# Performance work log

Hardware: AMD Instinct MI355X
Metric: run time of the kernel (lower is better)

## Reference

```python
import jax, jax.numpy as jnp
import numpy as np


def setup_inputs() -> dict:
    key = jax.random.key(0)
    k1, k2, k3, k4, k5, k6 = jax.random.split(key, 6)
    n_vars = 1000000
    n_constrs = 500000
    nnz = 20000000
    pred = jax.random.normal(k1, (n_vars,), dtype=jnp.float32)
    constr_idx = jax.random.randint(k2, (nnz,), 0, n_constrs, dtype=jnp.int32)
    var_idx = jax.random.randint(k3, (nnz,), 0, n_vars, dtype=jnp.int32)
    coeff = jax.random.normal(k4, (nnz,), dtype=jnp.float32)
    constr_rhs = jax.random.normal(k5, (n_constrs,), dtype=jnp.float32)
    constr_sense = jax.random.randint(k6, (n_constrs,), 1, 4, dtype=jnp.int32)  # 1=<=, 2=>=, 3===
    return {
        "pred": pred,
        "constr_idx": constr_idx,
        "var_idx": var_idx,
        "coeff": coeff,
        "constr_rhs": constr_rhs,
        "constr_sense": constr_sense,
        "n_vars": n_vars,
        "n_constrs": n_constrs,
    }


def reference(pred, constr_idx, var_idx, coeff, constr_rhs, constr_sense, n_vars, n_constrs):
    # probs = sigmoid(pred); ax[i] = sum over nnz entries of coeff * probs[var_idx]
    probs = jax.nn.sigmoid(pred)
    contrib = coeff * probs[var_idx]                      # [nnz]
    ax = jax.ops.segment_sum(contrib, constr_idx, num_segments=n_constrs)  # [n_constrs]
    le = jax.nn.relu(ax - constr_rhs)      # sense == 1 (<=)
    ge = jax.nn.relu(constr_rhs - ax)      # sense == 2 (>=)
    eq = jnp.abs(ax - constr_rhs)          # sense == 3 (==)
    violations = jnp.where(constr_sense == 1, le,
                  jnp.where(constr_sense == 2, ge,
                   jnp.where(constr_sense == 3, eq, jnp.zeros_like(ax))))
    return violations.mean()  # reduction='mean'
```

## Files before the change

### kernel.cpp

```cpp
#include <hip/hip_runtime.h>
#include <math.h>

#define R_LOG2 13
#define R_BKT  8192
#define SLICE  8
#define MAXNB  64
#define PB     512
#define BLK_RECS 8192

typedef int      iv4 __attribute__((ext_vector_type(4)));
typedef float    fv4 __attribute__((ext_vector_type(4)));
typedef unsigned uv4 __attribute__((ext_vector_type(4)));

__device__ __forceinline__ unsigned short f32_to_bf16_rne(float f) {
    unsigned b = __builtin_bit_cast(unsigned, f);
    b += 0x7FFFu + ((b >> 16) & 1u);
    return (unsigned short)(b >> 16);
}


__global__ void init_fast(const float4* __restrict__ pred4,
                          ushort4* __restrict__ probs4,
                          float4* __restrict__ ax4,
                          unsigned* __restrict__ cursor,
                          float* __restrict__ out,
                          int n_vars4, int nc4, int nb) {
    int i = blockIdx.x * blockDim.x + threadIdx.x;
    if (i < n_vars4) {
        float4 p = pred4[i];
        ushort4 q;
        q.x = f32_to_bf16_rne(1.0f / (1.0f + expf(-p.x)));
        q.y = f32_to_bf16_rne(1.0f / (1.0f + expf(-p.y)));
        q.z = f32_to_bf16_rne(1.0f / (1.0f + expf(-p.z)));
        q.w = f32_to_bf16_rne(1.0f / (1.0f + expf(-p.w)));
        probs4[i] = q;
    }
    if (i < nc4) ax4[i] = make_float4(0.f, 0.f, 0.f, 0.f);
    if (i < nb) cursor[i] = 0;
    if (i == 0) out[0] = 0.0f;
}

__global__ __launch_bounds__(PB) void partition_kernel(
        const int* __restrict__ cidx, const int* __restrict__ vidx,
        const float* __restrict__ coeff, const unsigned short* __restrict__ probs,
        unsigned* __restrict__ cursor, unsigned* __restrict__ recs,
        int nnz4, int nb, unsigned cap) {
    __shared__ unsigned sorted[BLK_RECS];
    __shared__ unsigned hist[8 * MAXNB];
    __shared__ unsigned lcur[8 * MAXNB];
    __shared__ unsigned bst[MAXNB + 1];
    __shared__ unsigned gbs[MAXNB];

    const int tid  = threadIdx.x;
    const int w    = tid >> 6;
    const int lane = tid & 63;

    hist[tid] = 0;

    unsigned rw[16];
    unsigned bk[16];
    bool     gv[4];
    const unsigned vbase = blockIdx.x * (BLK_RECS / 4);
    const bool full = (vbase + (BLK_RECS / 4)) <= (unsigned)nnz4;

    if (full) {
        #pragma unroll
        for (int g = 0; g < 4; ++g) {
            unsigned v = vbase + g * PB + (unsigned)tid;
            iv4 c4 = __builtin_nontemporal_load((const iv4*)cidx + v);
            iv4 v4 = __builtin_nontemporal_load((const iv4*)vidx + v);
            fv4 w4 = __builtin_nontemporal_load((const fv4*)coeff + v);
            int   cc[4] = {c4.x, c4.y, c4.z, c4.w};
            float vv[4] = {
                w4.x * __builtin_bit_cast(float, (unsigned)probs[v4.x] << 16),
                w4.y * __builtin_bit_cast(float, (unsigned)probs[v4.y] << 16),
                w4.z * __builtin_bit_cast(float, (unsigned)probs[v4.z] << 16),
                w4.w * __builtin_bit_cast(float, (unsigned)probs[v4.w] << 16)};
            #pragma unroll
            for (int j = 0; j < 4; ++j) {
                int k = g * 4 + j;
                unsigned bits = __builtin_bit_cast(unsigned, vv[j]);
                bits += 0x7FFFu + ((bits >> 16) & 1u);
                rw[k] = ((unsigned)(cc[j] & (R_BKT - 1)) << 16) | (bits >> 16);
                bk[k] = (unsigned)cc[j] >> R_LOG2;
            }
            gv[g] = true;
        }
    } else {
        #pragma unroll
        for (int g = 0; g < 4; ++g) {
            unsigned v = vbase + g * PB + (unsigned)tid;
            gv[g] = v < (unsigned)nnz4;
            if (gv[g]) {
                int4   c4 = ((const int4*)cidx)[v];
                int4   v4 = ((const int4*)vidx)[v];
                float4 w4 = ((const float4*)coeff)[v];
                int   cc[4] = {c4.x, c4.y, c4.z, c4.w};
                float vv[4] = {
                    w4.x * __builtin_bit_cast(float, (unsigned)probs[v4.x] << 16),
                    w4.y * __builtin_bit_cast(float, (unsigned)probs[v4.y] << 16),
                    w4.z * __builtin_bit_cast(float, (unsigned)probs[v4.z] << 16),
                    w4.w * __builtin_bit_cast(float, (unsigned)probs[v4.w] << 16)};
                #pragma unroll
                for (int j = 0; j < 4; ++j) {
                    int k = g * 4 + j;
                    unsigned bits = __builtin_bit_cast(unsigned, vv[j]);
                    bits += 0x7FFFu + ((bits >> 16) & 1u);
                    rw[k] = ((unsigned)(cc[j] & (R_BKT - 1)) << 16) | (bits >> 16);
                    bk[k] = (unsigned)cc[j] >> R_LOG2;
                }
            }
        }
    }
    __syncthreads();

    if (full) {
        #pragma unroll
        for (int k = 0; k < 16; ++k)
            atomicAdd(&hist[(w << 6) + bk[k]], 1u);
    } else {
        #pragma unroll
        for (int g = 0; g < 4; ++g) if (gv[g]) {
            #pragma unroll
            for (int j = 0; j < 4; ++j)
                atomicAdd(&hist[(w << 6) + bk[g * 4 + j]], 1u);
        }
    }
    __syncthreads();

    if (w == 0) {
        unsigned h[8];
        unsigned cnt = 0;
        if (lane < nb) {
            #pragma unroll
            for (int j = 0; j < 8; ++j) { h[j] = hist[(j << 6) + lane]; cnt += h[j]; }
        }
        unsigned sc = cnt;
        #pragma unroll
        for (int d = 1; d < 64; d <<= 1) {
            unsigned t = __shfl_up(sc, d, 64);
            if (lane >= d) sc += t;
        }
        unsigned excl  = sc - cnt;
        unsigned total = __shfl(sc, nb - 1, 64);
        if (lane < nb) {
            bst[lane] = excl;
            unsigned run = excl;
            #pragma unroll
            for (int j = 0; j < 8; ++j) { lcur[(j << 6) + lane] = run; run += h[j]; }
            gbs[lane] = cnt ? atomicAdd(&cursor[lane], cnt) : 0u;
        }
        if (lane == 0) bst[nb] = total;
    }
    __syncthreads();

    if (full) {
        #pragma unroll
        for (int k = 0; k < 16; ++k) {
            unsigned pos = atomicAdd(&lcur[(w << 6) + bk[k]], 1u);
            sorted[pos] = rw[k];
        }
    } else {
        #pragma unroll
        for (int g = 0; g < 4; ++g) if (gv[g]) {
            #pragma unroll
            for (int j = 0; j < 4; ++j) {
                int k = g * 4 + j;
                unsigned pos = atomicAdd(&lcur[(w << 6) + bk[k]], 1u);
                sorted[pos] = rw[k];
            }
        }
    }
    __syncthreads();

    for (int b = w; b < nb; b += 8) {
        unsigned st = bst[b], en = bst[b + 1], gb = gbs[b];
        unsigned* dst = recs + (size_t)b * cap;
        for (unsigned p = st + (unsigned)lane; p < en; p += 64u) {
            unsigned pos = gb + (p - st);
            if (pos < cap) __builtin_nontemporal_store(sorted[p], &dst[pos]);
        }
    }
}

__global__ __launch_bounds__(256) void accum_kernel(
        const unsigned* __restrict__ recs, const unsigned* __restrict__ cursor,
        float* __restrict__ ax, int n_constrs, unsigned cap) {
    __shared__ float acc[R_BKT];
    const int b = blockIdx.x / SLICE;
    const int s = blockIdx.x % SLICE;
    for (int j = threadIdx.x * 4; j < R_BKT; j += blockDim.x * 4)
        *(float4*)(acc + j) = make_float4(0.f, 0.f, 0.f, 0.f);
    __syncthreads();

    unsigned cnt = cursor[b];
    if (cnt > cap) cnt = cap;
    const unsigned* base = recs + (size_t)b * cap;

    unsigned c4 = cnt >> 2;
    unsigned s4 = (unsigned)(((unsigned long long)c4 * s) / SLICE);
    unsigned e4 = (unsigned)(((unsigned long long)c4 * (s + 1)) / SLICE);
    const uv4* b4 = (const uv4*)base;
    #pragma unroll 2
    for (unsigned i = s4 + threadIdx.x; i < e4; i += blockDim.x) {
        uv4 r = __builtin_nontemporal_load(b4 + i);
        unsafeAtomicAdd(&acc[r.x >> 16], __builtin_bit_cast(float, (r.x & 0xFFFFu) << 16));
        unsafeAtomicAdd(&acc[r.y >> 16], __builtin_bit_cast(float, (r.y & 0xFFFFu) << 16));
        unsafeAtomicAdd(&acc[r.z >> 16], __builtin_bit_cast(float, (r.z & 0xFFFFu) << 16));
        unsafeAtomicAdd(&acc[r.w >> 16], __builtin_bit_cast(float, (r.w & 0xFFFFu) << 16));
    }
    if (s == SLICE - 1) {
        for (unsigned i = (c4 << 2) + threadIdx.x; i < cnt; i += blockDim.x) {
            unsigned r = base[i];
            unsafeAtomicAdd(&acc[r >> 16], __builtin_bit_cast(float, (r & 0xFFFFu) << 16));
        }
    }
    __syncthreads();

    const int gb = b * R_BKT;
    for (int j = threadIdx.x; j < R_BKT; j += blockDim.x) {
        int g = gb + j;
        if (g < n_constrs)
            unsafeAtomicAdd(&ax[g], acc[j]);
    }
}

__device__ __forceinline__ float viol(float d, int sn) {
    return (sn == 1) ? fmaxf(d, 0.0f)
         : (sn == 2) ? fmaxf(-d, 0.0f)
         : (sn == 3) ? fabsf(d)
         : 0.0f;
}

__global__ void reduce_fast(const float4* __restrict__ ax4,
                            const float4* __restrict__ rhs4,
                            const int4* __restrict__ sense4,
                            float* __restrict__ out,
                            int n4, float inv_n) {
    int i = blockIdx.x * blockDim.x + threadIdx.x;
    float v = 0.0f;
    if (i < n4) {
        float4 a = ax4[i];
        float4 r = rhs4[i];
        int4  sn = sense4[i];
        v = viol(a.x - r.x, sn.x) + viol(a.y - r.y, sn.y)
          + viol(a.z - r.z, sn.z) + viol(a.w - r.w, sn.w);
    }
    #pragma unroll
    for (int off = 32; off > 0; off >>= 1)
        v += __shfl_down(v, off, 64);
    __shared__ float wsum[4];
    int lane = threadIdx.x & 63;
    int wid  = threadIdx.x >> 6;
    if (lane == 0) wsum[wid] = v;
    __syncthreads();
    if (threadIdx.x == 0)
        atomicAdd(out, (wsum[0] + wsum[1] + wsum[2] + wsum[3]) * inv_n);
}


__global__ void init_kernel(const float* __restrict__ pred,
                            float* __restrict__ probs,
                            float* __restrict__ ax,
                            float* __restrict__ out,
                            int n_vars, int n_constrs) {
    int i = blockIdx.x * blockDim.x + threadIdx.x;
    if (i < n_vars) probs[i] = 1.0f / (1.0f + expf(-pred[i]));
    if (i < n_constrs) ax[i] = 0.0f;
    if (i == 0) out[0] = 0.0f;
}

__global__ void scatter_kernel(const int* __restrict__ cidx,
                               const int* __restrict__ vidx,
                               const float* __restrict__ coeff,
                               const float* __restrict__ probs,
                               float* __restrict__ ax,
                               int nnz) {
    int i = blockIdx.x * blockDim.x + threadIdx.x;
    long long base = (long long)i * 4;
    if (base + 3 < (long long)nnz) {
        int4   c = ((const int4*)cidx)[i];
        int4   v = ((const int4*)vidx)[i];
        float4 w = ((const float4*)coeff)[i];
        unsafeAtomicAdd(&ax[c.x], w.x * probs[v.x]);
        unsafeAtomicAdd(&ax[c.y], w.y * probs[v.y]);
        unsafeAtomicAdd(&ax[c.z], w.z * probs[v.z]);
        unsafeAtomicAdd(&ax[c.w], w.w * probs[v.w]);
    } else if (base < (long long)nnz) {
        for (long long k = base; k < (long long)nnz; ++k)
            unsafeAtomicAdd(&ax[cidx[k]], coeff[k] * probs[vidx[k]]);
    }
}

__global__ void reduce_kernel(const float* __restrict__ ax,
                              const float* __restrict__ rhs,
                              const int* __restrict__ sense,
                              float* __restrict__ out,
                              int n_constrs, float inv_n) {
    int i = blockIdx.x * blockDim.x + threadIdx.x;
    float v = 0.0f;
    if (i < n_constrs) {
        float d = ax[i] - rhs[i];
        int s = sense[i];
        v = (s == 1) ? fmaxf(d, 0.0f)
          : (s == 2) ? fmaxf(-d, 0.0f)
          : (s == 3) ? fabsf(d)
          : 0.0f;
    }
    #pragma unroll
    for (int off = 32; off > 0; off >>= 1)
        v += __shfl_down(v, off, 64);
    __shared__ float wsum[4];
    int lane = threadIdx.x & 63;
    int wid  = threadIdx.x >> 6;
    if (lane == 0) wsum[wid] = v;
    __syncthreads();
    if (threadIdx.x == 0)
        atomicAdd(out, (wsum[0] + wsum[1] + wsum[2] + wsum[3]) * inv_n);
}


static inline size_t align16(size_t x) { return (x + 15) & ~(size_t)15; }

extern "C" void kernel_launch(void* const* d_in, const int* in_sizes, int n_in,
                              void* d_out, int out_size, void* d_ws, size_t ws_size,
                              hipStream_t stream) {
    const float* pred  = (const float*)d_in[0];
    const int*   cidx  = (const int*)d_in[1];
    const int*   vidx  = (const int*)d_in[2];
    const float* coeff = (const float*)d_in[3];
    const float* rhs   = (const float*)d_in[4];
    const int*   sense = (const int*)d_in[5];

    const int n_vars    = in_sizes[0];
    const int nnz       = in_sizes[1];
    const int n_constrs = in_sizes[4];
    const int B = 256;
    const float inv_n = 1.0f / (float)n_constrs;

    const int nb = (n_constrs + R_BKT - 1) / R_BKT;
    unsigned cap = (unsigned)(((double)nnz * R_BKT / (double)n_constrs) * 1.0625) + 1024;
    cap = (cap + 3u) & ~3u;

    size_t off_probs  = 0;
    size_t off_cursor = align16(off_probs + (size_t)n_vars * 2);
    size_t off_recs   = align16(off_cursor + (size_t)nb * 4);
    size_t off_ax     = align16(off_recs + (size_t)nb * cap * 4);
    size_t need_fast  = off_ax + (size_t)n_constrs * 4;

    bool fast = (ws_size >= need_fast) && (nb <= MAXNB) && ((nnz & 3) == 0)
             && ((n_vars & 3) == 0) && ((n_constrs & 3) == 0);

    if (fast) {
        unsigned short* probs  = (unsigned short*)((char*)d_ws + off_probs);
        unsigned*       cursor = (unsigned*)((char*)d_ws + off_cursor);
        unsigned*       recs   = (unsigned*)((char*)d_ws + off_recs);
        float*          ax     = (float*)((char*)d_ws + off_ax);
        float*          out    = (float*)d_out;

        int n_vars4 = n_vars >> 2;
        int nc4     = n_constrs >> 2;
        int init_n  = n_vars4 > nc4 ? n_vars4 : nc4;
        if (init_n < nb) init_n = nb;
        init_fast<<<(init_n + B - 1) / B, B, 0, stream>>>(
            (const float4*)pred, (ushort4*)probs, (float4*)ax, cursor, out,
            n_vars4, nc4, nb);

        int nnz4 = nnz >> 2;
        int nblk1 = (nnz4 + (BLK_RECS / 4) - 1) / (BLK_RECS / 4);
        partition_kernel<<<nblk1, PB, 0, stream>>>(
            cidx, vidx, coeff, probs, cursor, recs, nnz4, nb, cap);

        accum_kernel<<<nb * SLICE, B, 0, stream>>>(
            recs, cursor, ax, n_constrs, cap);

        reduce_fast<<<(nc4 + B - 1) / B, B, 0, stream>>>(
            (const float4*)ax, (const float4*)rhs, (const int4*)sense,
            out, nc4, inv_n);
    } else {
        float* probs = (float*)d_ws;
        float* ax    = probs + n_vars;
        float* out   = (float*)d_out;

        int init_n = n_vars > n_constrs ? n_vars : n_constrs;
        init_kernel<<<(init_n + B - 1) / B, B, 0, stream>>>(
            pred, probs, ax, out, n_vars, n_constrs);

        int n_vec_threads = (nnz + 3) / 4;
        scatter_kernel<<<(n_vec_threads + B - 1) / B, B, 0, stream>>>(
            cidx, vidx, coeff, probs, ax, nnz);

        reduce_kernel<<<(n_constrs + B - 1) / B, B, 0, stream>>>(
            ax, rhs, sense, out, n_constrs, inv_n);
    }
}
```

Baseline: 447.4 us.

## Stripe bucket cursors across partition blocks and reorder loads around histogram

Bucket cursors and record regions are split into 8 stripes chosen by block index, so global atomic contention on each bucket cursor is spread across stripes. Each accum block now owns one whole stripe rather than a slice of a shared bucket. The partition kernel loads constraint indices first, packs bucket ids into bytes to save registers, and builds the histogram before loading vidx/coeff and gathering probs, overlapping the gather latency with LDS atomics. A second warp issues the global cursor atomics in parallel with the first warp's scan. The risk is per-stripe capacity overflow, since capacity is now computed per stripe with less statistical slack.

```diff
diff --git a/kernel.cpp b/kernel.cpp
--- a/kernel.cpp
+++ b/kernel.cpp
@@ -3,7 +3,7 @@
 
 #define R_LOG2 13
 #define R_BKT  8192
-#define SLICE  8
+#define NSTRIPE 8
 #define MAXNB  64
 #define PB     512
 #define BLK_RECS 8192
@@ -24,7 +24,7 @@
                           float4* __restrict__ ax4,
                           unsigned* __restrict__ cursor,
                           float* __restrict__ out,
-                          int n_vars4, int nc4, int nb) {
+                          int n_vars4, int nc4) {
     int i = blockIdx.x * blockDim.x + threadIdx.x;
     if (i < n_vars4) {
         float4 p = pred4[i];
@@ -36,7 +36,7 @@
         probs4[i] = q;
     }
     if (i < nc4) ax4[i] = make_float4(0.f, 0.f, 0.f, 0.f);
-    if (i < nb) cursor[i] = 0;
+    if (i < MAXNB * NSTRIPE) cursor[i] = 0;
     if (i == 0) out[0] = 0.0f;
 }
 
@@ -44,7 +44,7 @@
         const int* __restrict__ cidx, const int* __restrict__ vidx,
         const float* __restrict__ coeff, const unsigned short* __restrict__ probs,
         unsigned* __restrict__ cursor, unsigned* __restrict__ recs,
-        int nnz4, int nb, unsigned cap) {
+        int nnz4, int nb, unsigned scap) {
     __shared__ unsigned sorted[BLK_RECS];
     __shared__ unsigned hist[8 * MAXNB];
     __shared__ unsigned lcur[8 * MAXNB];
@@ -54,11 +54,12 @@
     const int tid  = threadIdx.x;
     const int w    = tid >> 6;
     const int lane = tid & 63;
+    const int rep  = blockIdx.x & (NSTRIPE - 1);
 
     hist[tid] = 0;
 
     unsigned rw[16];
-    unsigned bk[16];
+    unsigned bkp[4];
     bool     gv[4];
     const unsigned vbase = blockIdx.x * (BLK_RECS / 4);
     const bool full = (vbase + (BLK_RECS / 4)) <= (unsigned)nnz4;
@@ -68,22 +69,14 @@
         for (int g = 0; g < 4; ++g) {
             unsigned v = vbase + g * PB + (unsigned)tid;
             iv4 c4 = __builtin_nontemporal_load((const iv4*)cidx + v);
-            iv4 v4 = __builtin_nontemporal_load((const iv4*)vidx + v);
-            fv4 w4 = __builtin_nontemporal_load((const fv4*)coeff + v);
-            int   cc[4] = {c4.x, c4.y, c4.z, c4.w};
-            float vv[4] = {
-                w4.x * __builtin_bit_cast(float, (unsigned)probs[v4.x] << 16),
-                w4.y * __builtin_bit_cast(float, (unsigned)probs[v4.y] << 16),
-                w4.z * __builtin_bit_cast(float, (unsigned)probs[v4.z] << 16),
-                w4.w * __builtin_bit_cast(float, (unsigned)probs[v4.w] << 16)};
-            #pragma unroll
-            for (int j = 0; j < 4; ++j) {
-                int k = g * 4 + j;
-                unsigned bits = __builtin_bit_cast(unsigned, vv[j]);
-                bits += 0x7FFFu + ((bits >> 16) & 1u);
-                rw[k] = ((unsigned)(cc[j] & (R_BKT - 1)) << 16) | (bits >> 16);
-                bk[k] = (unsigned)cc[j] >> R_LOG2;
-            }
+            int cc[4] = {c4.x, c4.y, c4.z, c4.w};
+            bkp[g] = ((unsigned)cc[0] >> R_LOG2)
+                   | (((unsigned)cc[1] >> R_LOG2) << 8)
+                   | (((unsigned)cc[2] >> R_LOG2) << 16)
+                   | (((unsigned)cc[3] >> R_LOG2) << 24);
+            #pragma unroll
+            for (int j = 0; j < 4; ++j)
+                rw[g * 4 + j] = (unsigned)(cc[j] & (R_BKT - 1)) << 16;
             gv[g] = true;
         }
     } else {
@@ -91,24 +84,17 @@
         for (int g = 0; g < 4; ++g) {
             unsigned v = vbase + g * PB + (unsigned)tid;
             gv[g] = v < (unsigned)nnz4;
+            bkp[g] = 0;
             if (gv[g]) {
-                int4   c4 = ((const int4*)cidx)[v];
-                int4   v4 = ((const int4*)vidx)[v];
-                float4 w4 = ((const float4*)coeff)[v];
-                int   cc[4] = {c4.x, c4.y, c4.z, c4.w};
-                float vv[4] = {
-                    w4.x * __builtin_bit_cast(float, (unsigned)probs[v4.x] << 16),
-                    w4.y * __builtin_bit_cast(float, (unsigned)probs[v4.y] << 16),
-                    w4.z * __builtin_bit_cast(float, (unsigned)probs[v4.z] << 16),
-                    w4.w * __builtin_bit_cast(float, (unsigned)probs[v4.w] << 16)};
+                int4 c4 = ((const int4*)cidx)[v];
+                int cc[4] = {c4.x, c4.y, c4.z, c4.w};
+                bkp[g] = ((unsigned)cc[0] >> R_LOG2)
+                       | (((unsigned)cc[1] >> R_LOG2) << 8)
+                       | (((unsigned)cc[2] >> R_LOG2) << 16)
+                       | (((unsigned)cc[3] >> R_LOG2) << 24);
                 #pragma unroll
-                for (int j = 0; j < 4; ++j) {
-                    int k = g * 4 + j;
-                    unsigned bits = __builtin_bit_cast(unsigned, vv[j]);
-                    bits += 0x7FFFu + ((bits >> 16) & 1u);
-                    rw[k] = ((unsigned)(cc[j] & (R_BKT - 1)) << 16) | (bits >> 16);
-                    bk[k] = (unsigned)cc[j] >> R_LOG2;
-                }
+                for (int j = 0; j < 4; ++j)
+                    rw[g * 4 + j] = (unsigned)(cc[j] & (R_BKT - 1)) << 16;
             }
         }
     }
@@ -116,14 +102,50 @@
 
     if (full) {
         #pragma unroll
-        for (int k = 0; k < 16; ++k)
-            atomicAdd(&hist[(w << 6) + bk[k]], 1u);
+        for (int g = 0; g < 4; ++g)
+            #pragma unroll
+            for (int j = 0; j < 4; ++j)
+                atomicAdd(&hist[(w << 6) + ((bkp[g] >> (8 * j)) & 0xFFu)], 1u);
     } else {
         #pragma unroll
         for (int g = 0; g < 4; ++g) if (gv[g]) {
             #pragma unroll
             for (int j = 0; j < 4; ++j)
-                atomicAdd(&hist[(w << 6) + bk[g * 4 + j]], 1u);
+                atomicAdd(&hist[(w << 6) + ((bkp[g] >> (8 * j)) & 0xFFu)], 1u);
+        }
+    }
+
+    if (full) {
+        #pragma unroll
+        for (int g = 0; g < 4; ++g) {
+            unsigned v = vbase + g * PB + (unsigned)tid;
+            iv4 v4 = __builtin_nontemporal_load((const iv4*)vidx + v);
+            fv4 w4 = __builtin_nontemporal_load((const fv4*)coeff + v);
+            int   vi[4] = {v4.x, v4.y, v4.z, v4.w};
+            float wc[4] = {w4.x, w4.y, w4.z, w4.w};
+            #pragma unroll
+            for (int j = 0; j < 4; ++j) {
+                float pv = __builtin_bit_cast(float, (unsigned)probs[vi[j]] << 16);
+                unsigned bits = __builtin_bit_cast(unsigned, wc[j] * pv);
+                bits += 0x7FFFu + ((bits >> 16) & 1u);
+                rw[g * 4 + j] |= bits >> 16;
+            }
+        }
+    } else {
+        #pragma unroll
+        for (int g = 0; g < 4; ++g) if (gv[g]) {
+            unsigned v = vbase + g * PB + (unsigned)tid;
+            int4   v4 = ((const int4*)vidx)[v];
+            float4 w4 = ((const float4*)coeff)[v];
+            int   vi[4] = {v4.x, v4.y, v4.z, v4.w};
+            float wc[4] = {w4.x, w4.y, w4.z, w4.w};
+            #pragma unroll
+            for (int j = 0; j < 4; ++j) {
+                float pv = __builtin_bit_cast(float, (unsigned)probs[vi[j]] << 16);
+                unsigned bits = __builtin_bit_cast(unsigned, wc[j] * pv);
+                bits += 0x7FFFu + ((bits >> 16) & 1u);
+                rw[g * 4 + j] |= bits >> 16;
+            }
         }
     }
     __syncthreads();
@@ -148,26 +170,35 @@
             unsigned run = excl;
             #pragma unroll
             for (int j = 0; j < 8; ++j) { lcur[(j << 6) + lane] = run; run += h[j]; }
-            gbs[lane] = cnt ? atomicAdd(&cursor[lane], cnt) : 0u;
         }
         if (lane == 0) bst[nb] = total;
+    } else if (w == 1) {
+        if (lane < nb) {
+            unsigned cnt2 = 0;
+            #pragma unroll
+            for (int j = 0; j < 8; ++j) cnt2 += hist[(j << 6) + lane];
+            gbs[lane] = cnt2 ? atomicAdd(&cursor[rep * MAXNB + lane], cnt2) : 0u;
+        }
     }
     __syncthreads();
 
     if (full) {
         #pragma unroll
-        for (int k = 0; k < 16; ++k) {
-            unsigned pos = atomicAdd(&lcur[(w << 6) + bk[k]], 1u);
-            sorted[pos] = rw[k];
-        }
+        for (int g = 0; g < 4; ++g)
+            #pragma unroll
+            for (int j = 0; j < 4; ++j) {
+                unsigned b = (bkp[g] >> (8 * j)) & 0xFFu;
+                unsigned pos = atomicAdd(&lcur[(w << 6) + b], 1u);
+                sorted[pos] = rw[g * 4 + j];
+            }
     } else {
         #pragma unroll
         for (int g = 0; g < 4; ++g) if (gv[g]) {
             #pragma unroll
             for (int j = 0; j < 4; ++j) {
-                int k = g * 4 + j;
-                unsigned pos = atomicAdd(&lcur[(w << 6) + bk[k]], 1u);
-                sorted[pos] = rw[k];
+                unsigned b = (bkp[g] >> (8 * j)) & 0xFFu;
+                unsigned pos = atomicAdd(&lcur[(w << 6) + b], 1u);
+                sorted[pos] = rw[g * 4 + j];
             }
         }
     }
@@ -175,45 +206,41 @@
 
     for (int b = w; b < nb; b += 8) {
         unsigned st = bst[b], en = bst[b + 1], gb = gbs[b];
-        unsigned* dst = recs + (size_t)b * cap;
+        unsigned* dst = recs + (size_t)(b * NSTRIPE + rep) * scap;
         for (unsigned p = st + (unsigned)lane; p < en; p += 64u) {
             unsigned pos = gb + (p - st);
-            if (pos < cap) __builtin_nontemporal_store(sorted[p], &dst[pos]);
+            if (pos < scap) __builtin_nontemporal_store(sorted[p], &dst[pos]);
         }
     }
 }
 
 __global__ __launch_bounds__(256) void accum_kernel(
         const unsigned* __restrict__ recs, const unsigned* __restrict__ cursor,
-        float* __restrict__ ax, int n_constrs, unsigned cap) {
+        float* __restrict__ ax, int n_constrs, unsigned scap) {
     __shared__ float acc[R_BKT];
-    const int b = blockIdx.x / SLICE;
-    const int s = blockIdx.x % SLICE;
+    const int b = blockIdx.x >> 3;
+    const int s = blockIdx.x & (NSTRIPE - 1);
     for (int j = threadIdx.x * 4; j < R_BKT; j += blockDim.x * 4)
         *(float4*)(acc + j) = make_float4(0.f, 0.f, 0.f, 0.f);
     __syncthreads();
 
-    unsigned cnt = cursor[b];
-    if (cnt > cap) cnt = cap;
-    const unsigned* base = recs + (size_t)b * cap;
+    unsigned cnt = cursor[s * MAXNB + b];
+    if (cnt > scap) cnt = scap;
+    const unsigned* base = recs + (size_t)(b * NSTRIPE + s) * scap;
 
     unsigned c4 = cnt >> 2;
-    unsigned s4 = (unsigned)(((unsigned long long)c4 * s) / SLICE);
-    unsigned e4 = (unsigned)(((unsigned long long)c4 * (s + 1)) / SLICE);
     const uv4* b4 = (const uv4*)base;
     #pragma unroll 2
-    for (unsigned i = s4 + threadIdx.x; i < e4; i += blockDim.x) {
+    for (unsigned i = threadIdx.x; i < c4; i += blockDim.x) {
         uv4 r = __builtin_nontemporal_load(b4 + i);
         unsafeAtomicAdd(&acc[r.x >> 16], __builtin_bit_cast(float, (r.x & 0xFFFFu) << 16));
         unsafeAtomicAdd(&acc[r.y >> 16], __builtin_bit_cast(float, (r.y & 0xFFFFu) << 16));
         unsafeAtomicAdd(&acc[r.z >> 16], __builtin_bit_cast(float, (r.z & 0xFFFFu) << 16));
         unsafeAtomicAdd(&acc[r.w >> 16], __builtin_bit_cast(float, (r.w & 0xFFFFu) << 16));
     }
-    if (s == SLICE - 1) {
-        for (unsigned i = (c4 << 2) + threadIdx.x; i < cnt; i += blockDim.x) {
-            unsigned r = base[i];
-            unsafeAtomicAdd(&acc[r >> 16], __builtin_bit_cast(float, (r & 0xFFFFu) << 16));
-        }
+    for (unsigned i = (c4 << 2) + threadIdx.x; i < cnt; i += blockDim.x) {
+        unsigned r = base[i];
+        unsafeAtomicAdd(&acc[r >> 16], __builtin_bit_cast(float, (r & 0xFFFFu) << 16));
     }
     __syncthreads();
 
@@ -339,13 +366,14 @@
     const float inv_n = 1.0f / (float)n_constrs;
 
     const int nb = (n_constrs + R_BKT - 1) / R_BKT;
-    unsigned cap = (unsigned)(((double)nnz * R_BKT / (double)n_constrs) * 1.0625) + 1024;
-    cap = (cap + 3u) & ~3u;
+    unsigned scap = (unsigned)(((double)nnz * R_BKT / (double)n_constrs / NSTRIPE)
+                               * 1.0625) + 1024;
+    scap = (scap + 3u) & ~3u;
 
     size_t off_probs  = 0;
     size_t off_cursor = align16(off_probs + (size_t)n_vars * 2);
-    size_t off_recs   = align16(off_cursor + (size_t)nb * 4);
-    size_t off_ax     = align16(off_recs + (size_t)nb * cap * 4);
+    size_t off_recs   = align16(off_cursor + (size_t)MAXNB * NSTRIPE * 4);
+    size_t off_ax     = align16(off_recs + (size_t)nb * NSTRIPE * scap * 4);
     size_t need_fast  = off_ax + (size_t)n_constrs * 4;
 
     bool fast = (ws_size >= need_fast) && (nb <= MAXNB) && ((nnz & 3) == 0)
@@ -361,18 +389,18 @@
         int n_vars4 = n_vars >> 2;
         int nc4     = n_constrs >> 2;
         int init_n  = n_vars4 > nc4 ? n_vars4 : nc4;
-        if (init_n < nb) init_n = nb;
+        if (init_n < MAXNB * NSTRIPE) init_n = MAXNB * NSTRIPE;
         init_fast<<<(init_n + B - 1) / B, B, 0, stream>>>(
             (const float4*)pred, (ushort4*)probs, (float4*)ax, cursor, out,
-            n_vars4, nc4, nb);
+            n_vars4, nc4);
 
         int nnz4 = nnz >> 2;
         int nblk1 = (nnz4 + (BLK_RECS / 4) - 1) / (BLK_RECS / 4);
         partition_kernel<<<nblk1, PB, 0, stream>>>(
-            cidx, vidx, coeff, probs, cursor, recs, nnz4, nb, cap);
-
-        accum_kernel<<<nb * SLICE, B, 0, stream>>>(
-            recs, cursor, ax, n_constrs, cap);
+            cidx, vidx, coeff, probs, cursor, recs, nnz4, nb, scap);
+
+        accum_kernel<<<nb * NSTRIPE, B, 0, stream>>>(
+            recs, cursor, ax, n_constrs, scap);
 
         reduce_fast<<<(nc4 + B - 1) / B, B, 0, stream>>>(
             (const float4*)ax, (const float4*)rhs, (const int4*)sense,
```

Measured after the change: 439.2 us. Within noise of the previous version (-1.8%).
